# Optimization experiments

Hardware: AMD Instinct MI355X
Metric: run time of the kernel (lower is better)

The kernel has to match this reference:

```python
import jax, jax.numpy as jnp
import numpy as np

E, IN, OUT, T = 8, 2048, 5632, 16384
_GROUP_SIZES = np.array([1024, 3072, 512, 4096, 2048, 1536, 2560, 1536])  # sums to T


def setup_inputs() -> dict:
    key = jax.random.key(0)
    k1, k2 = jax.random.split(key)
    x = jax.random.normal(k1, (T, IN), dtype=jnp.float32)
    # Expert weights [num_experts, out_features, in_features], kaiming-ish scale
    weight = jax.random.normal(k2, (E, OUT, IN), dtype=jnp.float32) * (1.0 / np.sqrt(IN))
    offsets = jnp.asarray(np.concatenate([[0], np.cumsum(_GROUP_SIZES)]), dtype=jnp.int32)
    return {"input": x, "weight": weight, "expert_offsets": offsets}


def reference(input, weight, expert_offsets):
    """Grouped GEMM: output[s_i:e_i] = input[s_i:e_i] @ weight[i].T (bias=None).

    Tokens are pre-sorted by expert; expert_offsets [E+1] gives each expert's
    contiguous token range. Offsets are routing metadata (static w.r.t. math),
    so we read them as concrete ints and loop over the small fixed expert set.
    """
    offs = np.asarray(jax.device_get(expert_offsets))
    num_experts = weight.shape[0]
    outs = []
    for i in range(num_experts):
        s, e = int(offs[i]), int(offs[i + 1])
        # [m_i, in] @ [in, out] -> [m_i, out]
        outs.append(input[s:e] @ weight[i].T)
    return jnp.concatenate(outs, axis=0)  # [total_tokens, out_features]
```

## Files before the change

### kernel.cpp

```cpp
#include <hip/hip_runtime.h>
#include <hip/hip_bf16.h>


#define T_TOK 16384
#define K_IN  2048
#define N_OUT 5632
#define NEXP  8

typedef __attribute__((ext_vector_type(8))) short short8;
typedef __attribute__((ext_vector_type(4))) float f32x4;
typedef unsigned short ushort_t;

__device__ __forceinline__ ushort_t f2bf(float x) {
  __hip_bfloat16 h = __float2bfloat16(x);
  return *reinterpret_cast<ushort_t*>(&h);
}

__global__ void __launch_bounds__(256) cvt2(const float* __restrict__ x,
                                            const float* __restrict__ w,
                                            ushort_t* __restrict__ ox,
                                            ushort_t* __restrict__ ow,
                                            int n8x, int n8t) {
  int i = blockIdx.x * blockDim.x + threadIdx.x;
  int stride = gridDim.x * blockDim.x;
  for (; i < n8t; i += stride) {
    const float* src;
    ushort_t* dst;
    int j;
    if (i < n8x) { src = x; dst = ox; j = i; }
    else         { src = w; dst = ow; j = i - n8x; }
    const float4* p = (const float4*)src + (size_t)j * 2;
    float4 a = p[0], b = p[1];
    short8 v;
    v[0] = (short)f2bf(a.x); v[1] = (short)f2bf(a.y);
    v[2] = (short)f2bf(a.z); v[3] = (short)f2bf(a.w);
    v[4] = (short)f2bf(b.x); v[5] = (short)f2bf(b.y);
    v[6] = (short)f2bf(b.z); v[7] = (short)f2bf(b.w);
    *((short8*)dst + j) = v;
  }
}

#define MT2 64
#define NT2 22
#define GRID2 (MT2 * NT2)

#define BAR() do { asm volatile("" ::: "memory"); \
                   __builtin_amdgcn_s_barrier(); \
                   asm volatile("" ::: "memory"); } while (0)
#define VMCNT(n) asm volatile("s_waitcnt vmcnt(" #n ")" ::: "memory")
#define LDF(p, imm) (*(const short8*)((p) + (imm)))

__device__ __forceinline__ void sgb_x() {
  __builtin_amdgcn_sched_group_barrier(0x010, 2, 0);
#pragma unroll
  for (int i = 0; i < 4; ++i) {
    __builtin_amdgcn_sched_group_barrier(0x008, 4, 0);
    __builtin_amdgcn_sched_group_barrier(0x100, 1, 0);
  }
}
__device__ __forceinline__ void sgb_y() {
  __builtin_amdgcn_sched_group_barrier(0x010, 2, 0);
  __builtin_amdgcn_sched_group_barrier(0x008, 16, 0);
}
__device__ __forceinline__ void sgb_z() {
  __builtin_amdgcn_sched_group_barrier(0x010, 2, 0);
#pragma unroll
  for (int i = 0; i < 8; ++i) {
    __builtin_amdgcn_sched_group_barrier(0x008, 2, 0);
    __builtin_amdgcn_sched_group_barrier(0x100, 2, 0);
  }
}

template <int M0>
__device__ __forceinline__ void mma_pair(f32x4 acc[8][4], const short8 a0[2],
                                         const short8 a1[2],
                                         const short8 bF[4][2]) {
  __builtin_amdgcn_s_setprio(1);
#pragma unroll
  for (int n = 0; n < 4; ++n)
#pragma unroll
    for (int s = 0; s < 2; ++s) {
      acc[M0][n] = __builtin_amdgcn_mfma_f32_16x16x32_bf16(a0[s], bF[n][s],
                                                           acc[M0][n], 0, 0, 0);
      acc[M0 + 1][n] = __builtin_amdgcn_mfma_f32_16x16x32_bf16(
          a1[s], bF[n][s], acc[M0 + 1][n], 0, 0, 0);
    }
  __builtin_amdgcn_s_setprio(0);
}

__global__ void __launch_bounds__(512, 2) gemm8(
    const ushort_t* __restrict__ abf, const ushort_t* __restrict__ wbf,
    const int* __restrict__ offs, float* __restrict__ out) {
  __shared__ __align__(16) ushort_t lds[2][2][2][8192];

  int bid = blockIdx.x;
  int loc = bid >> 3;
  int tn = loc >> 3;
  int tm = (bid & 7) * 8 + (loc & 7);

  const int t = threadIdx.x;
  const int w = t >> 6;
  const int l = t & 63;
  const int wm = w >> 2;
  const int wn = w & 3;

  const int row0 = tm * 256;
  int e = 0;
#pragma unroll
  for (int i = 1; i < NEXP; ++i) e += (row0 >= offs[i]) ? 1 : 0;

  const ushort_t* aB = abf + (size_t)row0 * K_IN;
  const ushort_t* wB =
      wbf + (size_t)e * N_OUT * K_IN + (size_t)(tn * 256) * K_IN;
  const size_t H = (size_t)128 * K_IN;

  const size_t srow = (size_t)(2 * w) * 8 + (l >> 3);
  const int scol = ((l & 7) ^ (l >> 3)) * 8;
  const ushort_t* const sA0 = aB + srow * K_IN + scol;
  const ushort_t* const sA1 = aB + (srow + 8) * K_IN + scol;
  const ushort_t* const sW0 = wB + srow * K_IN + scol;
  const ushort_t* const sW1 = wB + (srow + 8) * K_IN + scol;

  auto stage2 = [&](const ushort_t* s0, const ushort_t* s1, ushort_t* lreg,
                    size_t ko) {
    __builtin_amdgcn_global_load_lds(
        (const __attribute__((address_space(1))) void*)(s0 + ko),
        (__attribute__((address_space(3))) void*)(lreg + (2 * w) * 512), 16, 0, 0);
    __builtin_amdgcn_global_load_lds(
        (const __attribute__((address_space(1))) void*)(s1 + ko),
        (__attribute__((address_space(3))) void*)(lreg + (2 * w + 1) * 512), 16, 0, 0);
  };

  f32x4 acc[8][4];
#pragma unroll
  for (int i = 0; i < 8; ++i)
#pragma unroll
    for (int j = 0; j < 4; ++j)
#pragma unroll
      for (int r = 0; r < 4; ++r) acc[i][j][r] = 0.f;

  const int l15 = l & 15;
  const int kgo2 = (l >> 4) * 16;
  const int swz = (l15 & 7) << 4;
  const int fo0 = l15 * 128 + (kgo2 ^ swz);
  const int fo1 = l15 * 128 + ((64 + kgo2) ^ swz);
  const char* aP[2][2];
  const char* bP[2][2];
#pragma unroll
  for (int b = 0; b < 2; ++b) {
    aP[b][0] = (const char*)&lds[b][0][wm][0] + fo0;
    aP[b][1] = (const char*)&lds[b][0][wm][0] + fo1;
    bP[b][0] = (const char*)&lds[b][1][wn >> 1][0] + (wn & 1) * 8192 + fo0;
    bP[b][1] = (const char*)&lds[b][1][wn >> 1][0] + (wn & 1) * 8192 + fo1;
  }

#define LDA_PAIR(d0, d1, buf, m)                          \
  do {                                                    \
    d0[0] = LDF(aP[buf][0], (m) * 2048);                  \
    d0[1] = LDF(aP[buf][1], (m) * 2048);                  \
    d1[0] = LDF(aP[buf][0], ((m) + 1) * 2048);            \
    d1[1] = LDF(aP[buf][1], ((m) + 1) * 2048);            \
  } while (0)
#define LDB_ALL(dst, buf)                                 \
  do {                                                    \
    _Pragma("unroll")                                     \
    for (int n = 0; n < 4; ++n) {                         \
      dst[n][0] = LDF(bP[buf][0], n * 2048);              \
      dst[n][1] = LDF(bP[buf][1], n * 2048);              \
    }                                                     \
  } while (0)

  stage2(sA0, sA1, &lds[0][0][0][0], 0);
  stage2(sA0, sA1, &lds[0][0][1][0], H);
  stage2(sW0, sW1, &lds[0][1][0][0], 0);
  stage2(sW0, sW1, &lds[0][1][1][0], H);
  stage2(sW0, sW1, &lds[1][1][0][0], 64);
  stage2(sW0, sW1, &lds[1][1][1][0], H + 64);
  stage2(sA0, sA1, &lds[1][0][0][0], 64);
  VMCNT(6);
  BAR();

  short8 bF[4][2];
  short8 r0a[2], r0b[2];
  short8 r1a[2], r1b[2];
  LDB_ALL(bF, 0);
  LDA_PAIR(r0a, r0b, 0, 0);
  LDA_PAIR(r1a, r1b, 0, 2);

#pragma unroll 1
  for (int J = 0; J < 15; ++J) {
    const size_t kO1 = (size_t)(2 * J + 1) * 64;
    const size_t kO2 = (size_t)(2 * J + 2) * 64;
    const size_t kO3 = (size_t)(2 * J + 3) * 64;

    sgb_x();
    mma_pair<0>(acc, r0a, r0b, bF);
    stage2(sA0, sA1, &lds[1][0][1][0], H + kO1);
    LDA_PAIR(r0a, r0b, 0, 4);
    BAR();
    sgb_x();
    mma_pair<2>(acc, r1a, r1b, bF);
    stage2(sW0, sW1, &lds[0][1][0][0], kO2);
    LDA_PAIR(r1a, r1b, 0, 6);
    BAR();
    sgb_y();
    mma_pair<4>(acc, r0a, r0b, bF);
    stage2(sW0, sW1, &lds[0][1][1][0], H + kO2);
    VMCNT(4);
    BAR();
    sgb_z();
    mma_pair<6>(acc, r1a, r1b, bF);
    LDB_ALL(bF, 1);
    LDA_PAIR(r0a, r0b, 1, 0);
    stage2(sA0, sA1, &lds[0][0][0][0], kO2);
    LDA_PAIR(r1a, r1b, 1, 2);
    BAR();
    sgb_x();
    mma_pair<0>(acc, r0a, r0b, bF);
    stage2(sA0, sA1, &lds[0][0][1][0], H + kO2);
    LDA_PAIR(r0a, r0b, 1, 4);
    BAR();
    sgb_x();
    mma_pair<2>(acc, r1a, r1b, bF);
    stage2(sW0, sW1, &lds[1][1][0][0], kO3);
    LDA_PAIR(r1a, r1b, 1, 6);
    BAR();
    sgb_y();
    mma_pair<4>(acc, r0a, r0b, bF);
    stage2(sW0, sW1, &lds[1][1][1][0], H + kO3);
    VMCNT(4);
    BAR();
    sgb_z();
    mma_pair<6>(acc, r1a, r1b, bF);
    LDB_ALL(bF, 0);
    LDA_PAIR(r0a, r0b, 0, 0);
    stage2(sA0, sA1, &lds[1][0][0][0], kO3);
    LDA_PAIR(r1a, r1b, 0, 2);
    BAR();
  }

  {
    sgb_x();
    mma_pair<0>(acc, r0a, r0b, bF);
    stage2(sA0, sA1, &lds[1][0][1][0], H + 1984);
    LDA_PAIR(r0a, r0b, 0, 4);
    BAR();
    sgb_x();
    mma_pair<2>(acc, r1a, r1b, bF);
    LDA_PAIR(r1a, r1b, 0, 6);
    BAR();
    sgb_y();
    mma_pair<4>(acc, r0a, r0b, bF);
    VMCNT(0);
    BAR();
    sgb_z();
    mma_pair<6>(acc, r1a, r1b, bF);
    LDB_ALL(bF, 1);
    LDA_PAIR(r0a, r0b, 1, 0);
    LDA_PAIR(r1a, r1b, 1, 2);
    BAR();
    sgb_x();
    mma_pair<0>(acc, r0a, r0b, bF);
    LDA_PAIR(r0a, r0b, 1, 4);
    BAR();
    sgb_x();
    mma_pair<2>(acc, r1a, r1b, bF);
    LDA_PAIR(r1a, r1b, 1, 6);
    BAR();
    sgb_y();
    mma_pair<4>(acc, r0a, r0b, bF);
    BAR();
    mma_pair<6>(acc, r1a, r1b, bF);
  }

  const int cr = (l >> 4) * 4;
  const int cc = l & 15;
  float* ob = out + (size_t)(row0 + wm * 128) * N_OUT + tn * 256 + wn * 64;
#pragma unroll
  for (int m = 0; m < 8; ++m)
#pragma unroll
    for (int n = 0; n < 4; ++n)
#pragma unroll
      for (int r = 0; r < 4; ++r)
        ob[(size_t)(m * 16 + cr + r) * N_OUT + n * 16 + cc] = acc[m][n][r];
#undef LDA_PAIR
#undef LDB_ALL
}

#define BM 128
#define BN 128
#define BK 64
#define MT (T_TOK / BM)
#define NTILE (N_OUT / BN)

__global__ void __launch_bounds__(256) gemm_fb(const float* __restrict__ af,
                                               const float* __restrict__ wf,
                                               const int* __restrict__ offs,
                                               float* __restrict__ out) {
  __shared__ __align__(16) ushort_t lsA[BM * BK];
  __shared__ __align__(16) ushort_t lsB[BN * BK];
  int bid = blockIdx.x;
  int wg = (bid & 7) * ((MT * NTILE) >> 3) + (bid >> 3);
  int tm = wg / NTILE, tn = wg - tm * NTILE;
  const int t = threadIdx.x, w = t >> 6, l = t & 63;
  const int row0 = tm * BM;
  int e = 0;
#pragma unroll
  for (int i = 1; i < NEXP; ++i) e += (row0 >= offs[i]) ? 1 : 0;
  const size_t wbase = (size_t)e * ((size_t)N_OUT * K_IN);
  f32x4 acc[4][4];
#pragma unroll
  for (int i = 0; i < 4; ++i)
#pragma unroll
    for (int j = 0; j < 4; ++j)
#pragma unroll
      for (int r = 0; r < 4; ++r) acc[i][j][r] = 0.f;
  const int wm = w >> 1, wn = w & 1;
  const int rA = wm * 64 + (l & 15), rB = wn * 64 + (l & 15);
  const int kgo = (l >> 4) * 8;
  for (int kt = 0; kt < K_IN / BK; ++kt) {
    const int k0 = kt * BK;
    if (kt) __syncthreads();
#pragma unroll
    for (int p = 0; p < 4; ++p) {
      const int ia = (p * 4 + w) * 64 + l;
      const float4* g = (const float4*)(af + (size_t)(row0 + (ia >> 3)) * K_IN +
                                        k0 + (ia & 7) * 8);
      float4 a = g[0], b = g[1];
      short8 v;
      v[0] = (short)f2bf(a.x); v[1] = (short)f2bf(a.y);
      v[2] = (short)f2bf(a.z); v[3] = (short)f2bf(a.w);
      v[4] = (short)f2bf(b.x); v[5] = (short)f2bf(b.y);
      v[6] = (short)f2bf(b.z); v[7] = (short)f2bf(b.w);
      *(short8*)&lsA[ia * 8] = v;
    }
#pragma unroll
    for (int p = 0; p < 4; ++p) {
      const int ib = (p * 4 + w) * 64 + l;
      const float4* g = (const float4*)(wf + wbase +
                                        (size_t)(tn * BN + (ib >> 3)) * K_IN +
                                        k0 + (ib & 7) * 8);
      float4 a = g[0], b = g[1];
      short8 v;
      v[0] = (short)f2bf(a.x); v[1] = (short)f2bf(a.y);
      v[2] = (short)f2bf(a.z); v[3] = (short)f2bf(a.w);
      v[4] = (short)f2bf(b.x); v[5] = (short)f2bf(b.y);
      v[6] = (short)f2bf(b.z); v[7] = (short)f2bf(b.w);
      *(short8*)&lsB[ib * 8] = v;
    }
    __syncthreads();
#pragma unroll
    for (int s = 0; s < 2; ++s) {
      const int ko = s * 32 + kgo;
      short8 aF[4], bFf[4];
#pragma unroll
      for (int i = 0; i < 4; ++i) aF[i] = *(const short8*)&lsA[(rA + i * 16) * BK + ko];
#pragma unroll
      for (int j = 0; j < 4; ++j) bFf[j] = *(const short8*)&lsB[(rB + j * 16) * BK + ko];
#pragma unroll
      for (int i = 0; i < 4; ++i)
#pragma unroll
        for (int j = 0; j < 4; ++j)
          acc[i][j] = __builtin_amdgcn_mfma_f32_16x16x32_bf16(aF[i], bFf[j],
                                                              acc[i][j], 0, 0, 0);
    }
  }
  const int cr = (l >> 4) * 4, cc = l & 15;
  float* ob = out + (size_t)(row0 + wm * 64) * N_OUT + tn * BN + wn * 64;
#pragma unroll
  for (int i = 0; i < 4; ++i)
#pragma unroll
    for (int j = 0; j < 4; ++j)
#pragma unroll
      for (int r = 0; r < 4; ++r)
        ob[(size_t)(i * 16 + cr + r) * N_OUT + j * 16 + cc] = acc[i][j][r];
}

extern "C" void kernel_launch(void* const* d_in, const int* in_sizes, int n_in,
                              void* d_out, int out_size, void* d_ws, size_t ws_size,
                              hipStream_t stream) {
  const float* x = (const float*)d_in[0];
  const float* wt = (const float*)d_in[1];
  const int* offs = (const int*)d_in[2];
  float* out = (float*)d_out;

  const size_t nA = (size_t)T_TOK * K_IN;
  const size_t nW = (size_t)NEXP * N_OUT * K_IN;
  const size_t need = (nA + nW) * sizeof(ushort_t);

  if (ws_size >= need) {
    ushort_t* abf = (ushort_t*)d_ws;
    ushort_t* wbf = abf + nA;
    cvt2<<<2048, 256, 0, stream>>>(x, wt, abf, wbf, (int)(nA / 8),
                                   (int)((nA + nW) / 8));
    gemm8<<<GRID2, 512, 0, stream>>>(abf, wbf, offs, out);
  } else {
    gemm_fb<<<MT * NTILE, 256, 0, stream>>>(x, wt, offs, out);
  }
}
```

Measured before the change: 477.7 us.

## Fuse fp32-to-bf16 conversion into GEMM via register-staged LDS pipeline

Drops the separate conversion kernel that wrote bf16 copies of the activations and all expert weights to workspace. The GEMM now loads fp32 tiles into registers, converts them to bf16 and writes them to LDS itself, replacing the direct global-to-LDS loads with a register-staged software pipeline and new scheduling groups. This removes one kernel launch and a full read-write pass over the converted data. In exchange the GEMM reads twice as many bytes per tile, has higher register pressure, and waits on LDS writes every stage.

After: 561.5 us. 1.18x slower.

```diff
diff --git a/kernel.cpp b/kernel.cpp
--- a/kernel.cpp
+++ b/kernel.cpp
@@ -16,28 +16,13 @@
   return *reinterpret_cast<ushort_t*>(&h);
 }
 
-__global__ void __launch_bounds__(256) cvt2(const float* __restrict__ x,
-                                            const float* __restrict__ w,
-                                            ushort_t* __restrict__ ox,
-                                            ushort_t* __restrict__ ow,
-                                            int n8x, int n8t) {
-  int i = blockIdx.x * blockDim.x + threadIdx.x;
-  int stride = gridDim.x * blockDim.x;
-  for (; i < n8t; i += stride) {
-    const float* src;
-    ushort_t* dst;
-    int j;
-    if (i < n8x) { src = x; dst = ox; j = i; }
-    else         { src = w; dst = ow; j = i - n8x; }
-    const float4* p = (const float4*)src + (size_t)j * 2;
-    float4 a = p[0], b = p[1];
-    short8 v;
-    v[0] = (short)f2bf(a.x); v[1] = (short)f2bf(a.y);
-    v[2] = (short)f2bf(a.z); v[3] = (short)f2bf(a.w);
-    v[4] = (short)f2bf(b.x); v[5] = (short)f2bf(b.y);
-    v[6] = (short)f2bf(b.z); v[7] = (short)f2bf(b.w);
-    *((short8*)dst + j) = v;
-  }
+__device__ __forceinline__ short8 cvt8(f32x4 a, f32x4 b) {
+  short8 v;
+  v[0] = (short)f2bf(a[0]); v[1] = (short)f2bf(a[1]);
+  v[2] = (short)f2bf(a[2]); v[3] = (short)f2bf(a[3]);
+  v[4] = (short)f2bf(b[0]); v[5] = (short)f2bf(b[1]);
+  v[6] = (short)f2bf(b[2]); v[7] = (short)f2bf(b[3]);
+  return v;
 }
 
 #define MT2 64
@@ -47,23 +32,26 @@
 #define BAR() do { asm volatile("" ::: "memory"); \
                    __builtin_amdgcn_s_barrier(); \
                    asm volatile("" ::: "memory"); } while (0)
-#define VMCNT(n) asm volatile("s_waitcnt vmcnt(" #n ")" ::: "memory")
+#define LGKM0() asm volatile("s_waitcnt lgkmcnt(0)" ::: "memory")
 #define LDF(p, imm) (*(const short8*)((p) + (imm)))
 
-__device__ __forceinline__ void sgb_x() {
-  __builtin_amdgcn_sched_group_barrier(0x010, 2, 0);
+__device__ __forceinline__ void sgb_a() {
+  __builtin_amdgcn_sched_group_barrier(0x020, 4, 0);
+  __builtin_amdgcn_sched_group_barrier(0x200, 2, 0);
 #pragma unroll
   for (int i = 0; i < 4; ++i) {
     __builtin_amdgcn_sched_group_barrier(0x008, 4, 0);
     __builtin_amdgcn_sched_group_barrier(0x100, 1, 0);
   }
 }
-__device__ __forceinline__ void sgb_y() {
-  __builtin_amdgcn_sched_group_barrier(0x010, 2, 0);
+__device__ __forceinline__ void sgb_b() {
+  __builtin_amdgcn_sched_group_barrier(0x020, 4, 0);
+  __builtin_amdgcn_sched_group_barrier(0x200, 2, 0);
   __builtin_amdgcn_sched_group_barrier(0x008, 16, 0);
 }
-__device__ __forceinline__ void sgb_z() {
-  __builtin_amdgcn_sched_group_barrier(0x010, 2, 0);
+__device__ __forceinline__ void sgb_c() {
+  __builtin_amdgcn_sched_group_barrier(0x020, 4, 0);
+  __builtin_amdgcn_sched_group_barrier(0x200, 2, 0);
 #pragma unroll
   for (int i = 0; i < 8; ++i) {
     __builtin_amdgcn_sched_group_barrier(0x008, 2, 0);
@@ -88,8 +76,8 @@
   __builtin_amdgcn_s_setprio(0);
 }
 
-__global__ void __launch_bounds__(512, 2) gemm8(
-    const ushort_t* __restrict__ abf, const ushort_t* __restrict__ wbf,
+__global__ void __launch_bounds__(512, 2) gemm_fused(
+    const float* __restrict__ xf, const float* __restrict__ wf,
     const int* __restrict__ offs, float* __restrict__ out) {
   __shared__ __align__(16) ushort_t lds[2][2][2][8192];
 
@@ -109,27 +97,30 @@
 #pragma unroll
   for (int i = 1; i < NEXP; ++i) e += (row0 >= offs[i]) ? 1 : 0;
 
-  const ushort_t* aB = abf + (size_t)row0 * K_IN;
-  const ushort_t* wB =
-      wbf + (size_t)e * N_OUT * K_IN + (size_t)(tn * 256) * K_IN;
   const size_t H = (size_t)128 * K_IN;
 
   const size_t srow = (size_t)(2 * w) * 8 + (l >> 3);
   const int scol = ((l & 7) ^ (l >> 3)) * 8;
-  const ushort_t* const sA0 = aB + srow * K_IN + scol;
-  const ushort_t* const sA1 = aB + (srow + 8) * K_IN + scol;
-  const ushort_t* const sW0 = wB + srow * K_IN + scol;
-  const ushort_t* const sW1 = wB + (srow + 8) * K_IN + scol;
-
-  auto stage2 = [&](const ushort_t* s0, const ushort_t* s1, ushort_t* lreg,
-                    size_t ko) {
-    __builtin_amdgcn_global_load_lds(
-        (const __attribute__((address_space(1))) void*)(s0 + ko),
-        (__attribute__((address_space(3))) void*)(lreg + (2 * w) * 512), 16, 0, 0);
-    __builtin_amdgcn_global_load_lds(
-        (const __attribute__((address_space(1))) void*)(s1 + ko),
-        (__attribute__((address_space(3))) void*)(lreg + (2 * w + 1) * 512), 16, 0, 0);
-  };
+  const float* const fA0 = xf + ((size_t)row0 + srow) * K_IN + scol;
+  const float* const fA1 = fA0 + (size_t)8 * K_IN;
+  const float* const fW0 =
+      wf + (size_t)e * N_OUT * K_IN + ((size_t)(tn * 256) + srow) * K_IN + scol;
+  const float* const fW1 = fW0 + (size_t)8 * K_IN;
+
+  f32x4 L0[4], L1[4];
+#define LOADSET(L, p0, p1, ko) do {                 \
+    L[0] = *(const f32x4*)((p0) + (ko));            \
+    L[1] = *(const f32x4*)((p0) + (ko) + 4);        \
+    L[2] = *(const f32x4*)((p1) + (ko));            \
+    L[3] = *(const f32x4*)((p1) + (ko) + 4);        \
+  } while (0)
+#define WRITESET(L, dreg) do {                      \
+    short8 v0_ = cvt8(L[0], L[1]);                  \
+    short8 v1_ = cvt8(L[2], L[3]);                  \
+    ushort_t* d_ = (dreg) + 2 * w * 512 + l * 8;    \
+    *(short8*)d_ = v0_;                             \
+    *(short8*)(d_ + 512) = v1_;                     \
+  } while (0)
 
   f32x4 acc[8][4];
 #pragma unroll
@@ -170,14 +161,15 @@
     }                                                     \
   } while (0)
 
-  stage2(sA0, sA1, &lds[0][0][0][0], 0);
-  stage2(sA0, sA1, &lds[0][0][1][0], H);
-  stage2(sW0, sW1, &lds[0][1][0][0], 0);
-  stage2(sW0, sW1, &lds[0][1][1][0], H);
-  stage2(sW0, sW1, &lds[1][1][0][0], 64);
-  stage2(sW0, sW1, &lds[1][1][1][0], H + 64);
-  stage2(sA0, sA1, &lds[1][0][0][0], 64);
-  VMCNT(6);
+  LOADSET(L0, fA0, fA1, 0);
+  LOADSET(L1, fA0, fA1, H);
+  WRITESET(L0, &lds[0][0][0][0]); LOADSET(L0, fW0, fW1, 0);
+  WRITESET(L1, &lds[0][0][1][0]); LOADSET(L1, fW0, fW1, H);
+  WRITESET(L0, &lds[0][1][0][0]); LOADSET(L0, fW0, fW1, 64);
+  WRITESET(L1, &lds[0][1][1][0]); LOADSET(L1, fW0, fW1, H + 64);
+  WRITESET(L0, &lds[1][1][0][0]); LOADSET(L0, fA0, fA1, 64);
+  WRITESET(L1, &lds[1][1][1][0]);
+  LGKM0();
   BAR();
 
   short8 bF[4][2];
@@ -193,83 +185,91 @@
     const size_t kO2 = (size_t)(2 * J + 2) * 64;
     const size_t kO3 = (size_t)(2 * J + 3) * 64;
 
-    sgb_x();
+    WRITESET(L0, &lds[1][0][0][0]);
+    LOADSET(L1, fA0, fA1, H + kO1);
+    sgb_a();
     mma_pair<0>(acc, r0a, r0b, bF);
-    stage2(sA0, sA1, &lds[1][0][1][0], H + kO1);
     LDA_PAIR(r0a, r0b, 0, 4);
-    BAR();
-    sgb_x();
-    mma_pair<2>(acc, r1a, r1b, bF);
-    stage2(sW0, sW1, &lds[0][1][0][0], kO2);
-    LDA_PAIR(r1a, r1b, 0, 6);
-    BAR();
-    sgb_y();
-    mma_pair<4>(acc, r0a, r0b, bF);
-    stage2(sW0, sW1, &lds[0][1][1][0], H + kO2);
-    VMCNT(4);
-    BAR();
-    sgb_z();
-    mma_pair<6>(acc, r1a, r1b, bF);
-    LDB_ALL(bF, 1);
-    LDA_PAIR(r0a, r0b, 1, 0);
-    stage2(sA0, sA1, &lds[0][0][0][0], kO2);
-    LDA_PAIR(r1a, r1b, 1, 2);
-    BAR();
-    sgb_x();
-    mma_pair<0>(acc, r0a, r0b, bF);
-    stage2(sA0, sA1, &lds[0][0][1][0], H + kO2);
-    LDA_PAIR(r0a, r0b, 1, 4);
-    BAR();
-    sgb_x();
-    mma_pair<2>(acc, r1a, r1b, bF);
-    stage2(sW0, sW1, &lds[1][1][0][0], kO3);
-    LDA_PAIR(r1a, r1b, 1, 6);
-    BAR();
-    sgb_y();
-    mma_pair<4>(acc, r0a, r0b, bF);
-    stage2(sW0, sW1, &lds[1][1][1][0], H + kO3);
-    VMCNT(4);
-    BAR();
-    sgb_z();
-    mma_pair<6>(acc, r1a, r1b, bF);
-    LDB_ALL(bF, 0);
-    LDA_PAIR(r0a, r0b, 0, 0);
-    stage2(sA0, sA1, &lds[1][0][0][0], kO3);
-    LDA_PAIR(r1a, r1b, 0, 2);
-    BAR();
-  }
-
-  {
-    sgb_x();
-    mma_pair<0>(acc, r0a, r0b, bF);
-    stage2(sA0, sA1, &lds[1][0][1][0], H + 1984);
-    LDA_PAIR(r0a, r0b, 0, 4);
-    BAR();
-    sgb_x();
+    LGKM0(); BAR();
+    WRITESET(L1, &lds[1][0][1][0]);
+    LOADSET(L0, fW0, fW1, kO2);
+    sgb_a();
     mma_pair<2>(acc, r1a, r1b, bF);
     LDA_PAIR(r1a, r1b, 0, 6);
-    BAR();
-    sgb_y();
+    LGKM0(); BAR();
+    WRITESET(L0, &lds[0][1][0][0]);
+    LOADSET(L1, fW0, fW1, H + kO2);
+    sgb_b();
     mma_pair<4>(acc, r0a, r0b, bF);
-    VMCNT(0);
-    BAR();
-    sgb_z();
+    LGKM0(); BAR();
+    WRITESET(L1, &lds[0][1][1][0]);
+    LOADSET(L0, fA0, fA1, kO2);
+    sgb_c();
     mma_pair<6>(acc, r1a, r1b, bF);
     LDB_ALL(bF, 1);
     LDA_PAIR(r0a, r0b, 1, 0);
     LDA_PAIR(r1a, r1b, 1, 2);
-    BAR();
-    sgb_x();
+    LGKM0(); BAR();
+    WRITESET(L0, &lds[0][0][0][0]);
+    LOADSET(L1, fA0, fA1, H + kO2);
+    sgb_a();
     mma_pair<0>(acc, r0a, r0b, bF);
     LDA_PAIR(r0a, r0b, 1, 4);
-    BAR();
-    sgb_x();
+    LGKM0(); BAR();
+    WRITESET(L1, &lds[0][0][1][0]);
+    LOADSET(L0, fW0, fW1, kO3);
+    sgb_a();
     mma_pair<2>(acc, r1a, r1b, bF);
     LDA_PAIR(r1a, r1b, 1, 6);
-    BAR();
-    sgb_y();
+    LGKM0(); BAR();
+    WRITESET(L0, &lds[1][1][0][0]);
+    LOADSET(L1, fW0, fW1, H + kO3);
+    sgb_b();
     mma_pair<4>(acc, r0a, r0b, bF);
-    BAR();
+    LGKM0(); BAR();
+    WRITESET(L1, &lds[1][1][1][0]);
+    LOADSET(L0, fA0, fA1, kO3);
+    sgb_c();
+    mma_pair<6>(acc, r1a, r1b, bF);
+    LDB_ALL(bF, 0);
+    LDA_PAIR(r0a, r0b, 0, 0);
+    LDA_PAIR(r1a, r1b, 0, 2);
+    LGKM0(); BAR();
+  }
+
+  {
+    WRITESET(L0, &lds[1][0][0][0]);
+    LOADSET(L1, fA0, fA1, H + 1984);
+    sgb_a();
+    mma_pair<0>(acc, r0a, r0b, bF);
+    LDA_PAIR(r0a, r0b, 0, 4);
+    LGKM0(); BAR();
+
+    WRITESET(L1, &lds[1][0][1][0]);
+    mma_pair<2>(acc, r1a, r1b, bF);
+    LDA_PAIR(r1a, r1b, 0, 6);
+    LGKM0(); BAR();
+
+    mma_pair<4>(acc, r0a, r0b, bF);
+    BAR();
+
+    mma_pair<6>(acc, r1a, r1b, bF);
+    LDB_ALL(bF, 1);
+    LDA_PAIR(r0a, r0b, 1, 0);
+    LDA_PAIR(r1a, r1b, 1, 2);
+    BAR();
+
+    mma_pair<0>(acc, r0a, r0b, bF);
+    LDA_PAIR(r0a, r0b, 1, 4);
+    BAR();
+
+    mma_pair<2>(acc, r1a, r1b, bF);
+    LDA_PAIR(r1a, r1b, 1, 6);
+    BAR();
+
+    mma_pair<4>(acc, r0a, r0b, bF);
+    BAR();
+
     mma_pair<6>(acc, r1a, r1b, bF);
   }
 
@@ -285,95 +285,8 @@
         ob[(size_t)(m * 16 + cr + r) * N_OUT + n * 16 + cc] = acc[m][n][r];
 #undef LDA_PAIR
 #undef LDB_ALL
-}
-
-#define BM 128
-#define BN 128
-#define BK 64
-#define MT (T_TOK / BM)
-#define NTILE (N_OUT / BN)
-
-__global__ void __launch_bounds__(256) gemm_fb(const float* __restrict__ af,
-                                               const float* __restrict__ wf,
-                                               const int* __restrict__ offs,
-                                               float* __restrict__ out) {
-  __shared__ __align__(16) ushort_t lsA[BM * BK];
-  __shared__ __align__(16) ushort_t lsB[BN * BK];
-  int bid = blockIdx.x;
-  int wg = (bid & 7) * ((MT * NTILE) >> 3) + (bid >> 3);
-  int tm = wg / NTILE, tn = wg - tm * NTILE;
-  const int t = threadIdx.x, w = t >> 6, l = t & 63;
-  const int row0 = tm * BM;
-  int e = 0;
-#pragma unroll
-  for (int i = 1; i < NEXP; ++i) e += (row0 >= offs[i]) ? 1 : 0;
-  const size_t wbase = (size_t)e * ((size_t)N_OUT * K_IN);
-  f32x4 acc[4][4];
-#pragma unroll
-  for (int i = 0; i < 4; ++i)
-#pragma unroll
-    for (int j = 0; j < 4; ++j)
-#pragma unroll
-      for (int r = 0; r < 4; ++r) acc[i][j][r] = 0.f;
-  const int wm = w >> 1, wn = w & 1;
-  const int rA = wm * 64 + (l & 15), rB = wn * 64 + (l & 15);
-  const int kgo = (l >> 4) * 8;
-  for (int kt = 0; kt < K_IN / BK; ++kt) {
-    const int k0 = kt * BK;
-    if (kt) __syncthreads();
-#pragma unroll
-    for (int p = 0; p < 4; ++p) {
-      const int ia = (p * 4 + w) * 64 + l;
-      const float4* g = (const float4*)(af + (size_t)(row0 + (ia >> 3)) * K_IN +
-                                        k0 + (ia & 7) * 8);
-      float4 a = g[0], b = g[1];
-      short8 v;
-      v[0] = (short)f2bf(a.x); v[1] = (short)f2bf(a.y);
-      v[2] = (short)f2bf(a.z); v[3] = (short)f2bf(a.w);
-      v[4] = (short)f2bf(b.x); v[5] = (short)f2bf(b.y);
-      v[6] = (short)f2bf(b.z); v[7] = (short)f2bf(b.w);
-      *(short8*)&lsA[ia * 8] = v;
-    }
-#pragma unroll
-    for (int p = 0; p < 4; ++p) {
-      const int ib = (p * 4 + w) * 64 + l;
-      const float4* g = (const float4*)(wf + wbase +
-                                        (size_t)(tn * BN + (ib >> 3)) * K_IN +
-                                        k0 + (ib & 7) * 8);
-      float4 a = g[0], b = g[1];
-      short8 v;
-      v[0] = (short)f2bf(a.x); v[1] = (short)f2bf(a.y);
-      v[2] = (short)f2bf(a.z); v[3] = (short)f2bf(a.w);
-      v[4] = (short)f2bf(b.x); v[5] = (short)f2bf(b.y);
-      v[6] = (short)f2bf(b.z); v[7] = (short)f2bf(b.w);
-      *(short8*)&lsB[ib * 8] = v;
-    }
-    __syncthreads();
-#pragma unroll
-    for (int s = 0; s < 2; ++s) {
-      const int ko = s * 32 + kgo;
-      short8 aF[4], bFf[4];
-#pragma unroll
-      for (int i = 0; i < 4; ++i) aF[i] = *(const short8*)&lsA[(rA + i * 16) * BK + ko];
-#pragma unroll
-      for (int j = 0; j < 4; ++j) bFf[j] = *(const short8*)&lsB[(rB + j * 16) * BK + ko];
-#pragma unroll
-      for (int i = 0; i < 4; ++i)
-#pragma unroll
-        for (int j = 0; j < 4; ++j)
-          acc[i][j] = __builtin_amdgcn_mfma_f32_16x16x32_bf16(aF[i], bFf[j],
-                                                              acc[i][j], 0, 0, 0);
-    }
-  }
-  const int cr = (l >> 4) * 4, cc = l & 15;
-  float* ob = out + (size_t)(row0 + wm * 64) * N_OUT + tn * BN + wn * 64;
-#pragma unroll
-  for (int i = 0; i < 4; ++i)
-#pragma unroll
-    for (int j = 0; j < 4; ++j)
-#pragma unroll
-      for (int r = 0; r < 4; ++r)
-        ob[(size_t)(i * 16 + cr + r) * N_OUT + j * 16 + cc] = acc[i][j][r];
+#undef LOADSET
+#undef WRITESET
 }
 
 extern "C" void kernel_launch(void* const* d_in, const int* in_sizes, int n_in,
@@ -383,18 +296,7 @@
   const float* wt = (const float*)d_in[1];
   const int* offs = (const int*)d_in[2];
   float* out = (float*)d_out;
-
-  const size_t nA = (size_t)T_TOK * K_IN;
-  const size_t nW = (size_t)NEXP * N_OUT * K_IN;
-  const size_t need = (nA + nW) * sizeof(ushort_t);
-
-  if (ws_size >= need) {
-    ushort_t* abf = (ushort_t*)d_ws;
-    ushort_t* wbf = abf + nA;
-    cvt2<<<2048, 256, 0, stream>>>(x, wt, abf, wbf, (int)(nA / 8),
-                                   (int)((nA + nW) / 8));
-    gemm8<<<GRID2, 512, 0, stream>>>(abf, wbf, offs, out);
-  } else {
-    gemm_fb<<<MT * NTILE, 256, 0, stream>>>(x, wt, offs, out);
-  }
-}
+  (void)d_ws; (void)ws_size;
+
+  gemm_fused<<<GRID2, 512, 0, stream>>>(x, wt, offs, out);
+}
```

## Switch main GEMM from 16x16x32 to 32x32x16 bf16 MFMA tiles

Applied to the files above, without the earlier changes.

Replaces the 16x16x32 MFMA instructions with 32x32x16 bf16 MFMAs, so each wave computes its 128x64 tile as 4x2 blocks of 32x32 accumulators. LDS fragment loads, swizzle offsets, scheduling group barriers and the output store layout are reworked to match the new fragment shape. The larger MFMA shape issues fewer instructions and fewer LDS reads per FLOP. The cost is different LDS access patterns that could cause bank conflicts, and a strided, less coalesced epilogue write.

Measured after the change: 533.2 us. 1.12x slower.

```diff
diff --git a/kernel.cpp b/kernel.cpp
--- a/kernel.cpp
+++ b/kernel.cpp
@@ -9,6 +9,7 @@
 
 typedef __attribute__((ext_vector_type(8))) short short8;
 typedef __attribute__((ext_vector_type(4))) float f32x4;
+typedef __attribute__((ext_vector_type(16))) float f32x16;
 typedef unsigned short ushort_t;
 
 __device__ __forceinline__ ushort_t f2bf(float x) {
@@ -48,43 +49,38 @@
                    __builtin_amdgcn_s_barrier(); \
                    asm volatile("" ::: "memory"); } while (0)
 #define VMCNT(n) asm volatile("s_waitcnt vmcnt(" #n ")" ::: "memory")
-#define LDF(p, imm) (*(const short8*)((p) + (imm)))
-
-__device__ __forceinline__ void sgb_x() {
+
+__device__ __forceinline__ void sgb_a() {
   __builtin_amdgcn_sched_group_barrier(0x010, 2, 0);
 #pragma unroll
   for (int i = 0; i < 4; ++i) {
-    __builtin_amdgcn_sched_group_barrier(0x008, 4, 0);
+    __builtin_amdgcn_sched_group_barrier(0x008, 2, 0);
     __builtin_amdgcn_sched_group_barrier(0x100, 1, 0);
   }
 }
-__device__ __forceinline__ void sgb_y() {
+__device__ __forceinline__ void sgb_b() {
   __builtin_amdgcn_sched_group_barrier(0x010, 2, 0);
-  __builtin_amdgcn_sched_group_barrier(0x008, 16, 0);
-}
-__device__ __forceinline__ void sgb_z() {
+  __builtin_amdgcn_sched_group_barrier(0x008, 8, 0);
+}
+__device__ __forceinline__ void sgb_c() {
   __builtin_amdgcn_sched_group_barrier(0x010, 2, 0);
 #pragma unroll
   for (int i = 0; i < 8; ++i) {
-    __builtin_amdgcn_sched_group_barrier(0x008, 2, 0);
+    __builtin_amdgcn_sched_group_barrier(0x008, 1, 0);
     __builtin_amdgcn_sched_group_barrier(0x100, 2, 0);
   }
 }
 
-template <int M0>
-__device__ __forceinline__ void mma_pair(f32x4 acc[8][4], const short8 a0[2],
-                                         const short8 a1[2],
-                                         const short8 bF[4][2]) {
+template <int M>
+__device__ __forceinline__ void mma_q(f32x16 acc[4][2], const short8 aF[4],
+                                      const short8 bF[2][4]) {
   __builtin_amdgcn_s_setprio(1);
 #pragma unroll
-  for (int n = 0; n < 4; ++n)
-#pragma unroll
-    for (int s = 0; s < 2; ++s) {
-      acc[M0][n] = __builtin_amdgcn_mfma_f32_16x16x32_bf16(a0[s], bF[n][s],
-                                                           acc[M0][n], 0, 0, 0);
-      acc[M0 + 1][n] = __builtin_amdgcn_mfma_f32_16x16x32_bf16(
-          a1[s], bF[n][s], acc[M0 + 1][n], 0, 0, 0);
-    }
+  for (int q = 0; q < 4; ++q)
+#pragma unroll
+    for (int n = 0; n < 2; ++n)
+      acc[M][n] = __builtin_amdgcn_mfma_f32_32x32x16_bf16(aF[q], bF[n][q],
+                                                          acc[M][n], 0, 0, 0);
   __builtin_amdgcn_s_setprio(0);
 }
 
@@ -131,43 +127,41 @@
         (__attribute__((address_space(3))) void*)(lreg + (2 * w + 1) * 512), 16, 0, 0);
   };
 
-  f32x4 acc[8][4];
-#pragma unroll
-  for (int i = 0; i < 8; ++i)
-#pragma unroll
-    for (int j = 0; j < 4; ++j)
-#pragma unroll
-      for (int r = 0; r < 4; ++r) acc[i][j][r] = 0.f;
-
-  const int l15 = l & 15;
-  const int kgo2 = (l >> 4) * 16;
-  const int swz = (l15 & 7) << 4;
-  const int fo0 = l15 * 128 + (kgo2 ^ swz);
-  const int fo1 = l15 * 128 + ((64 + kgo2) ^ swz);
-  const char* aP[2][2];
-  const char* bP[2][2];
+  f32x16 acc[4][2];
+#pragma unroll
+  for (int i = 0; i < 4; ++i)
+#pragma unroll
+    for (int j = 0; j < 2; ++j)
+#pragma unroll
+      for (int r = 0; r < 16; ++r) acc[i][j][r] = 0.f;
+
+  const int kh = (l >> 5) * 16;
+  const int swz = (l & 7) << 4;
+  int offq[4];
+#pragma unroll
+  for (int q = 0; q < 4; ++q) offq[q] = (q * 32 + kh) ^ swz;
+  const char* aBs[2];
+  const char* bBs[2];
 #pragma unroll
   for (int b = 0; b < 2; ++b) {
-    aP[b][0] = (const char*)&lds[b][0][wm][0] + fo0;
-    aP[b][1] = (const char*)&lds[b][0][wm][0] + fo1;
-    bP[b][0] = (const char*)&lds[b][1][wn >> 1][0] + (wn & 1) * 8192 + fo0;
-    bP[b][1] = (const char*)&lds[b][1][wn >> 1][0] + (wn & 1) * 8192 + fo1;
-  }
-
-#define LDA_PAIR(d0, d1, buf, m)                          \
-  do {                                                    \
-    d0[0] = LDF(aP[buf][0], (m) * 2048);                  \
-    d0[1] = LDF(aP[buf][1], (m) * 2048);                  \
-    d1[0] = LDF(aP[buf][0], ((m) + 1) * 2048);            \
-    d1[1] = LDF(aP[buf][1], ((m) + 1) * 2048);            \
+    aBs[b] = (const char*)&lds[b][0][wm][0] + (l & 31) * 128;
+    bBs[b] = (const char*)&lds[b][1][wn >> 1][0] + (wn & 1) * 8192 +
+             (l & 31) * 128;
+  }
+
+#define LDA_Q(dst, buf, m)                                        \
+  do {                                                            \
+    _Pragma("unroll")                                             \
+    for (int q = 0; q < 4; ++q)                                   \
+      dst[q] = *(const short8*)(aBs[buf] + (m) * 4096 + offq[q]); \
   } while (0)
-#define LDB_ALL(dst, buf)                                 \
-  do {                                                    \
-    _Pragma("unroll")                                     \
-    for (int n = 0; n < 4; ++n) {                         \
-      dst[n][0] = LDF(bP[buf][0], n * 2048);              \
-      dst[n][1] = LDF(bP[buf][1], n * 2048);              \
-    }                                                     \
+#define LDB_Q(dst, buf)                                                 \
+  do {                                                                  \
+    _Pragma("unroll")                                                   \
+    for (int q = 0; q < 4; ++q)                                         \
+      _Pragma("unroll")                                                 \
+      for (int n = 0; n < 2; ++n)                                       \
+        dst[n][q] = *(const short8*)(bBs[buf] + (n) * 4096 + offq[q]);  \
   } while (0)
 
   stage2(sA0, sA1, &lds[0][0][0][0], 0);
@@ -180,12 +174,11 @@
   VMCNT(6);
   BAR();
 
-  short8 bF[4][2];
-  short8 r0a[2], r0b[2];
-  short8 r1a[2], r1b[2];
-  LDB_ALL(bF, 0);
-  LDA_PAIR(r0a, r0b, 0, 0);
-  LDA_PAIR(r1a, r1b, 0, 2);
+  short8 bF[2][4];
+  short8 R0[4], R1[4];
+  LDB_Q(bF, 0);
+  LDA_Q(R0, 0, 0);
+  LDA_Q(R1, 0, 1);
 
 #pragma unroll 1
   for (int J = 0; J < 15; ++J) {
@@ -193,98 +186,99 @@
     const size_t kO2 = (size_t)(2 * J + 2) * 64;
     const size_t kO3 = (size_t)(2 * J + 3) * 64;
 
-    sgb_x();
-    mma_pair<0>(acc, r0a, r0b, bF);
+    sgb_a();
+    mma_q<0>(acc, R0, bF);
     stage2(sA0, sA1, &lds[1][0][1][0], H + kO1);
-    LDA_PAIR(r0a, r0b, 0, 4);
-    BAR();
-    sgb_x();
-    mma_pair<2>(acc, r1a, r1b, bF);
+    LDA_Q(R0, 0, 2);
+    BAR();
+    sgb_a();
+    mma_q<1>(acc, R1, bF);
     stage2(sW0, sW1, &lds[0][1][0][0], kO2);
-    LDA_PAIR(r1a, r1b, 0, 6);
-    BAR();
-    sgb_y();
-    mma_pair<4>(acc, r0a, r0b, bF);
+    LDA_Q(R1, 0, 3);
+    BAR();
+    sgb_b();
+    mma_q<2>(acc, R0, bF);
     stage2(sW0, sW1, &lds[0][1][1][0], H + kO2);
     VMCNT(4);
     BAR();
-    sgb_z();
-    mma_pair<6>(acc, r1a, r1b, bF);
-    LDB_ALL(bF, 1);
-    LDA_PAIR(r0a, r0b, 1, 0);
+    sgb_c();
+    mma_q<3>(acc, R1, bF);
+    LDB_Q(bF, 1);
+    LDA_Q(R0, 1, 0);
     stage2(sA0, sA1, &lds[0][0][0][0], kO2);
-    LDA_PAIR(r1a, r1b, 1, 2);
-    BAR();
-    sgb_x();
-    mma_pair<0>(acc, r0a, r0b, bF);
+    LDA_Q(R1, 1, 1);
+    BAR();
+    sgb_a();
+    mma_q<0>(acc, R0, bF);
     stage2(sA0, sA1, &lds[0][0][1][0], H + kO2);
-    LDA_PAIR(r0a, r0b, 1, 4);
-    BAR();
-    sgb_x();
-    mma_pair<2>(acc, r1a, r1b, bF);
+    LDA_Q(R0, 1, 2);
+    BAR();
+    sgb_a();
+    mma_q<1>(acc, R1, bF);
     stage2(sW0, sW1, &lds[1][1][0][0], kO3);
-    LDA_PAIR(r1a, r1b, 1, 6);
-    BAR();
-    sgb_y();
-    mma_pair<4>(acc, r0a, r0b, bF);
+    LDA_Q(R1, 1, 3);
+    BAR();
+    sgb_b();
+    mma_q<2>(acc, R0, bF);
     stage2(sW0, sW1, &lds[1][1][1][0], H + kO3);
     VMCNT(4);
     BAR();
-    sgb_z();
-    mma_pair<6>(acc, r1a, r1b, bF);
-    LDB_ALL(bF, 0);
-    LDA_PAIR(r0a, r0b, 0, 0);
+    sgb_c();
+    mma_q<3>(acc, R1, bF);
+    LDB_Q(bF, 0);
+    LDA_Q(R0, 0, 0);
     stage2(sA0, sA1, &lds[1][0][0][0], kO3);
-    LDA_PAIR(r1a, r1b, 0, 2);
+    LDA_Q(R1, 0, 1);
     BAR();
   }
 
   {
-    sgb_x();
-    mma_pair<0>(acc, r0a, r0b, bF);
+    sgb_a();
+    mma_q<0>(acc, R0, bF);
     stage2(sA0, sA1, &lds[1][0][1][0], H + 1984);
-    LDA_PAIR(r0a, r0b, 0, 4);
-    BAR();
-    sgb_x();
-    mma_pair<2>(acc, r1a, r1b, bF);
-    LDA_PAIR(r1a, r1b, 0, 6);
-    BAR();
-    sgb_y();
-    mma_pair<4>(acc, r0a, r0b, bF);
+    LDA_Q(R0, 0, 2);
+    BAR();
+    sgb_a();
+    mma_q<1>(acc, R1, bF);
+    LDA_Q(R1, 0, 3);
+    BAR();
+    sgb_b();
+    mma_q<2>(acc, R0, bF);
     VMCNT(0);
     BAR();
-    sgb_z();
-    mma_pair<6>(acc, r1a, r1b, bF);
-    LDB_ALL(bF, 1);
-    LDA_PAIR(r0a, r0b, 1, 0);
-    LDA_PAIR(r1a, r1b, 1, 2);
-    BAR();
-    sgb_x();
-    mma_pair<0>(acc, r0a, r0b, bF);
-    LDA_PAIR(r0a, r0b, 1, 4);
-    BAR();
-    sgb_x();
-    mma_pair<2>(acc, r1a, r1b, bF);
-    LDA_PAIR(r1a, r1b, 1, 6);
-    BAR();
-    sgb_y();
-    mma_pair<4>(acc, r0a, r0b, bF);
-    BAR();
-    mma_pair<6>(acc, r1a, r1b, bF);
-  }
-
-  const int cr = (l >> 4) * 4;
-  const int cc = l & 15;
+    sgb_c();
+    mma_q<3>(acc, R1, bF);
+    LDB_Q(bF, 1);
+    LDA_Q(R0, 1, 0);
+    LDA_Q(R1, 1, 1);
+    BAR();
+    sgb_a();
+    mma_q<0>(acc, R0, bF);
+    LDA_Q(R0, 1, 2);
+    BAR();
+    sgb_a();
+    mma_q<1>(acc, R1, bF);
+    LDA_Q(R1, 1, 3);
+    BAR();
+    sgb_b();
+    mma_q<2>(acc, R0, bF);
+    BAR();
+    mma_q<3>(acc, R1, bF);
+  }
+
+  const int cc = l & 31;
+  const int rb = 4 * (l >> 5);
   float* ob = out + (size_t)(row0 + wm * 128) * N_OUT + tn * 256 + wn * 64;
 #pragma unroll
-  for (int m = 0; m < 8; ++m)
-#pragma unroll
-    for (int n = 0; n < 4; ++n)
-#pragma unroll
-      for (int r = 0; r < 4; ++r)
-        ob[(size_t)(m * 16 + cr + r) * N_OUT + n * 16 + cc] = acc[m][n][r];
-#undef LDA_PAIR
-#undef LDB_ALL
+  for (int m = 0; m < 4; ++m)
+#pragma unroll
+    for (int n = 0; n < 2; ++n)
+#pragma unroll
+      for (int r = 0; r < 16; ++r)
+        ob[(size_t)(m * 32 + (r & 3) + 8 * (r >> 2) + rb) * N_OUT + n * 32 +
+           cc] = acc[m][n][r];
+#undef LDA_Q
+#undef LDB_Q
 }
 
 #define BM 128
```
